# Performance work log

Measured on AMD Instinct MI355X. Metric: run time of the kernel, lower is better.

Reference implementation:

```python
import math
import jax, jax.numpy as jnp
import numpy as np

SEQ_LEN = 2048
PATCH = 16
D_MODEL = 512
N_HEADS = 8
D_FF = 2048
E_LAYERS = 3
KERNELS = (8, 4, 2, 1)


def _pos_embedding(L, d):
    # standard sinusoidal PE, matches PositionalEmbedding
    pos = np.arange(L, dtype=np.float32)[:, None]
    div = np.exp(np.arange(0, d, 2, dtype=np.float32) * (-math.log(10000.0) / d))
    pe = np.zeros((L, d), dtype=np.float32)
    pe[:, 0::2] = np.sin(pos * div)
    pe[:, 1::2] = np.cos(pos * div)
    return jnp.asarray(pe)


def _layer_norm(x, g, b, eps=1e-5):
    mu = jnp.mean(x, axis=-1, keepdims=True)
    var = jnp.mean(jnp.square(x - mu), axis=-1, keepdims=True)
    return (x - mu) * jax.lax.rsqrt(var + eps) * g + b


def setup_inputs() -> dict:
    key = jax.random.key(0)
    ks = jax.random.split(key, 12)
    bs, c = 8, 32
    s = 0.02
    L, D = E_LAYERS, D_MODEL
    inp = {
        "x_enc": jax.random.normal(ks[0], (bs, SEQ_LEN, c), jnp.float32),
        "W_emb": jax.random.normal(ks[1], (PATCH, D), jnp.float32) * s,
        "Wq": jax.random.normal(ks[2], (L, D, D), jnp.float32) * s,
        "bq": jnp.zeros((L, D), jnp.float32),
        "Wk": jax.random.normal(ks[3], (L, D, D), jnp.float32) * s,
        "bk": jnp.zeros((L, D), jnp.float32),
        "Wv": jax.random.normal(ks[4], (L, D, D), jnp.float32) * s,
        "bv": jnp.zeros((L, D), jnp.float32),
        "Wo": jax.random.normal(ks[5], (L, D, D), jnp.float32) * s,
        "bo": jnp.zeros((L, D), jnp.float32),
        "ln1_g": jnp.ones((L, D), jnp.float32),
        "ln1_b": jnp.zeros((L, D), jnp.float32),
        "W1": jax.random.normal(ks[6], (L, D, D_FF), jnp.float32) * s,
        "b1": jnp.zeros((L, D_FF), jnp.float32),
        "W2": jax.random.normal(ks[7], (L, D_FF, D), jnp.float32) * s,
        "b2": jnp.zeros((L, D), jnp.float32),
        "ln2_g": jnp.ones((L, D), jnp.float32),
        "ln2_b": jnp.zeros((L, D), jnp.float32),
        "lnf_g": jnp.ones((D,), jnp.float32),
        "lnf_b": jnp.zeros((D,), jnp.float32),
    }
    return inp


def reference(x_enc, W_emb, Wq, bq, Wk, bk, Wv, bv, Wo, bo,
              ln1_g, ln1_b, W1, b1, W2, b2, ln2_g, ln2_b, lnf_g, lnf_b):
    bs, t, c = x_enc.shape
    B = bs * c
    # channel-independent sequences: (bs, t, c) -> (bs*c, t)
    x = jnp.transpose(x_enc, (0, 2, 1)).reshape(B, t)

    # multi-scale interval sampling + patch embedding per scale
    p_lens = [(t // k) // PATCH for k in KERNELS]  # [16, 32, 64, 128]
    toks = []
    for k in KERNELS:
        xs = x[:, ::k]  # interval sampling (replicate-pad unfold [...,0] == stride-k sampling here)
        patches = xs.reshape(B, -1, PATCH)  # non-overlapping patches (stride == patch_len)
        toks.append(patches @ W_emb)  # value embedding, no bias
    h = jnp.concatenate(toks, axis=1)  # (B, L_tot=240, D)

    # multi-scale positional embedding: downsample pe of finest scale
    pe = _pos_embedding(p_lens[-1], D_MODEL)
    pos = jnp.concatenate([pe[::k] for k in KERNELS], axis=0)  # (240, D)
    h = h + pos[None]

    # block-diagonal scale-independence mask
    seg = np.concatenate([np.full(pl, i, dtype=np.int32) for i, pl in enumerate(p_lens)])
    allowed = jnp.asarray(seg[:, None] == seg[None, :])  # (240, 240) True = attend

    hd = D_MODEL // N_HEADS
    scale = 1.0 / math.sqrt(hd)
    Ltot = h.shape[1]
    for i in range(E_LAYERS):
        q = (h @ Wq[i] + bq[i]).reshape(B, Ltot, N_HEADS, hd)
        k_ = (h @ Wk[i] + bk[i]).reshape(B, Ltot, N_HEADS, hd)
        v_ = (h @ Wv[i] + bv[i]).reshape(B, Ltot, N_HEADS, hd)
        scores = jnp.einsum('blhd,bmhd->bhlm', q, k_) * scale
        scores = jnp.where(allowed[None, None], scores, -jnp.inf)
        attn = jax.nn.softmax(scores, axis=-1)
        o = jnp.einsum('bhlm,bmhd->blhd', attn, v_).reshape(B, Ltot, D_MODEL)
        o = o @ Wo[i] + bo[i]
        h = _layer_norm(h + o, ln1_g[i], ln1_b[i])
        f = jax.nn.gelu(h @ W1[i] + b1[i]) @ W2[i] + b2[i]
        h = _layer_norm(h + f, ln2_g[i], ln2_b[i])
    return _layer_norm(h, lnf_g, lnf_b)
```

## Files before the change

kernel.cpp:

```cpp
#include <hip/hip_runtime.h>
#include <hip/hip_bf16.h>

typedef short bf16x8 __attribute__((ext_vector_type(8)));
typedef float f32x4 __attribute__((ext_vector_type(4)));
using bf16 = __hip_bfloat16;

#define GLOBAL_LOAD_LDS16(g, l)                                                          \
    __builtin_amdgcn_global_load_lds((const __attribute__((address_space(1))) unsigned int*)(g), \
                                     (__attribute__((address_space(3))) unsigned int*)(l), \
                                     16, 0, 0)

static __device__ __forceinline__ float gelu_f(float x) {
    float u = 1.5957691216057308f * x * (1.0f + 0.044715f * x * x);
    return x / (1.0f + __expf(-u));
}

static __device__ __forceinline__ unsigned pack_bf16(float lo, float hi) {
    union { bf16 h; unsigned short u; } a, b;
    a.h = __float2bfloat16(lo);
    b.h = __float2bfloat16(hi);
    return ((unsigned)b.u << 16) | (unsigned)a.u;
}

static __device__ __forceinline__ int eperm(int r) {
    return (r & 1) | (((r >> 2) & 3) << 1) | (((r >> 1) & 1) << 3);
}

__global__ __launch_bounds__(256) void transpose_f32_bf16(const float* __restrict__ in,
                                                          bf16* __restrict__ out,
                                                          int R, int C, size_t zso) {
    __shared__ float tile[32][33];
    size_t zi = (size_t)blockIdx.z * R * C;
    size_t zo = (size_t)blockIdx.z * zso;
    int c0 = blockIdx.x * 32, r0 = blockIdx.y * 32;
    int tx = threadIdx.x & 31, ty = threadIdx.x >> 5;
    #pragma unroll
    for (int i = 0; i < 32; i += 8) {
        int r = r0 + ty + i, c = c0 + tx;
        if (r < R && c < C) tile[ty + i][tx] = in[zi + (size_t)r * C + c];
    }
    __syncthreads();
    #pragma unroll
    for (int i = 0; i < 32; i += 8) {
        int c = c0 + ty + i, r = r0 + tx;
        if (c < C && r < R) out[zo + (size_t)c * R + r] = __float2bfloat16(tile[tx][ty + i]);
    }
}

__global__ __launch_bounds__(256) void concat_bias(const float* __restrict__ bq,
                                                   const float* __restrict__ bk,
                                                   const float* __restrict__ bv,
                                                   float* __restrict__ out) {
    int i = blockIdx.x * 256 + threadIdx.x;
    if (i < 3 * 1536) {
        int L = i / 1536, r = i - L * 1536;
        float v = (r < 512) ? bq[L * 512 + r]
                : (r < 1024) ? bk[L * 512 + r - 512]
                             : bv[L * 512 + r - 1024];
        out[i] = v;
    }
}

__global__ __launch_bounds__(256) void transpose_v(const bf16* __restrict__ in,
                                                   bf16* __restrict__ out) {
    __shared__ bf16 tile[32][33];
    int b = blockIdx.z;
    int d0 = blockIdx.x * 32, t0 = blockIdx.y * 32;
    int tx = threadIdx.x & 31, ty = threadIdx.x >> 5;
    #pragma unroll
    for (int i = 0; i < 32; i += 8) {
        int tt = t0 + ty + i, dd = d0 + tx;
        if (tt < 240) tile[ty + i][tx] = in[((size_t)b * 240 + tt) * 1536 + 1024 + dd];
    }
    __syncthreads();
    #pragma unroll
    for (int i = 0; i < 32; i += 8) {
        int dd = d0 + ty + i, tt = t0 + tx;
        if (tt < 240) out[((size_t)b * 512 + dd) * 240 + tt] = tile[tx][ty + i];
    }
}

__global__ __launch_bounds__(256) void embed_kernel(const float* __restrict__ x_enc,
                                                    const float* __restrict__ W_emb,
                                                    bf16* __restrict__ h) {
    int row = blockIdx.x;
    int b = row / 240, l = row - b * 240;
    int s = (l < 16) ? 0 : (l < 48) ? 1 : (l < 112) ? 2 : 3;
    int len = 16 << s;
    int off = len - 16;
    int kk = 8 >> s;
    int j = l - off;
    int bs_i = b >> 5, c_i = b & 31;
    __shared__ float xv[16];
    int t = threadIdx.x;
    if (t < 16) {
        int tau = (j * 16 + t) * kk;
        xv[t] = x_enc[((size_t)bs_i * 2048 + tau) * 32 + c_i];
    }
    __syncthreads();
    int pe_row = j * kk;
    const float NEG2LN = -0.035977892078032f;
    for (int d = t; d < 512; d += 256) {
        float acc = 0.f;
        #pragma unroll
        for (int i = 0; i < 16; ++i) acc += xv[i] * W_emb[i * 512 + d];
        int di = d >> 1;
        float ang = (float)pe_row * expf((float)di * NEG2LN);
        float pos = (d & 1) ? cosf(ang) : sinf(ang);
        h[(size_t)row * 512 + d] = __float2bfloat16(acc + pos);
    }
}

__global__ __launch_bounds__(256) void gemm_bt(const bf16* __restrict__ A,
                                               const bf16* __restrict__ Bt,
                                               const float* __restrict__ bias,
                                               bf16* __restrict__ C,
                                               int M, int N, int K, int act) {
    __shared__ __align__(16) bf16 smem[2 * 128 * 64];
    bf16* As = smem;
    bf16* Bs = smem + 128 * 64;
    const int t = threadIdx.x;
    const int wave = t >> 6, lane = t & 63;
    const int quad = lane >> 4, l16 = lane & 15;

    const int nwg = gridDim.x * gridDim.y;
    const int id = blockIdx.y * gridDim.x + blockIdx.x;
    const int swzb = (id & 7) * (nwg >> 3) + (id >> 3);
    const int bx = swzb % gridDim.x, by = swzb / gridDim.x;
    const int m0 = by * 128, n0 = bx * 128;
    const int wm = (wave >> 1) * 64, wn = (wave & 1) * 64;

    f32x4 acc[4][4];
    #pragma unroll
    for (int a = 0; a < 4; ++a)
        #pragma unroll
        for (int b = 0; b < 4; ++b)
            #pragma unroll
            for (int r = 0; r < 4; ++r) acc[a][b][r] = 0.0f;

    const int srow = lane >> 3;
    const int schunk = (lane & 7) ^ srow;
    const bf16* Abase = A + (size_t)(m0 + wave * 32 + srow) * K + schunk * 8;
    const bf16* Bbase = Bt + (size_t)(n0 + wave * 32 + srow) * K + schunk * 8;

    for (int k0 = 0; k0 < K; k0 += 64) {
        __syncthreads();
        #pragma unroll
        for (int p = 0; p < 4; ++p) {
            GLOBAL_LOAD_LDS16(Abase + (size_t)p * 8 * K + k0, As + (wave * 4 + p) * 512);
            GLOBAL_LOAD_LDS16(Bbase + (size_t)p * 8 * K + k0, Bs + (wave * 4 + p) * 512);
        }
        __syncthreads();
        #pragma unroll
        for (int kt = 0; kt < 2; ++kt) {
            bf16x8 af[4], bfr[4];
            #pragma unroll
            for (int mi = 0; mi < 4; ++mi) {
                int row = wm + mi * 16 + l16;
                af[mi] = *(const bf16x8*)(&As[row * 64 + (((kt << 2) + quad) ^ (l16 & 7)) * 8]);
            }
            #pragma unroll
            for (int ni = 0; ni < 4; ++ni) {
                int row = wn + ni * 16 + l16;
                bfr[ni] = *(const bf16x8*)(&Bs[row * 64 + (((kt << 2) + quad) ^ (l16 & 7)) * 8]);
            }
            #pragma unroll
            for (int mi = 0; mi < 4; ++mi)
                #pragma unroll
                for (int ni = 0; ni < 4; ++ni)
                    acc[mi][ni] = __builtin_amdgcn_mfma_f32_16x16x32_bf16(af[mi], bfr[ni],
                                                                         acc[mi][ni], 0, 0, 0);
        }
    }

    __syncthreads();
    {
        char* ctile = (char*)smem;
        const int oddl = l16 & 1;
        #pragma unroll
        for (int ni = 0; ni < 4; ++ni) {
            int colt = wn + ni * 16 + l16;
            float bv = bias[n0 + colt];
            #pragma unroll
            for (int mi = 0; mi < 4; ++mi) {
                float v0 = acc[mi][ni][0] + bv;
                float v1 = acc[mi][ni][1] + bv;
                float v2 = acc[mi][ni][2] + bv;
                float v3 = acc[mi][ni][3] + bv;
                if (act) {
                    v0 = gelu_f(v0); v1 = gelu_f(v1);
                    v2 = gelu_f(v2); v3 = gelu_f(v3);
                }
                float p0 = __shfl_xor(v0, 1);
                float p1 = __shfl_xor(v1, 1);
                float p2 = __shfl_xor(v2, 1);
                float p3 = __shfl_xor(v3, 1);
                float lo0 = oddl ? p1 : v0, hi0 = oddl ? v1 : p0;
                float lo1 = oddl ? p3 : v2, hi1 = oddl ? v3 : p2;
                int rowt0 = wm + mi * 16 + quad * 4 + oddl;
                int rowt1 = rowt0 + 2;
                int colp = colt & ~1;
                int ch = colp >> 3;
                *(unsigned*)(ctile + rowt0 * 256 + (((ch ^ eperm(rowt0)) << 4) | ((colp & 7) << 1)))
                    = pack_bf16(lo0, hi0);
                *(unsigned*)(ctile + rowt1 * 256 + (((ch ^ eperm(rowt1)) << 4) | ((colp & 7) << 1)))
                    = pack_bf16(lo1, hi1);
            }
        }
        __syncthreads();
        const int rsub = t >> 4;
        const int cch = t & 15;
        #pragma unroll
        for (int g = 0; g < 8; ++g) {
            int row = g * 16 + rsub;
            bf16x8 v = *(const bf16x8*)(ctile + row * 256 + ((cch ^ eperm(row)) << 4));
            *(bf16x8*)(C + (size_t)(m0 + row) * N + n0 + cch * 8) = v;
        }
    }
}

template<int LEN>
__global__ __launch_bounds__(256) void attn_mfma(const bf16* __restrict__ qkv,
                                                 const bf16* __restrict__ vt,
                                                 bf16* __restrict__ o) {
    constexpr int NT = LEN / 16;
    constexpr int KT = (LEN >= 32) ? (LEN / 32) : 1;
    constexpr int PST = (LEN == 16) ? 40 : (LEN + 8);
    constexpr int SLABS = LEN / 16;
    constexpr int OFF = LEN - 16;
    __shared__ __align__(16) bf16 Plds[4 * 16 * PST];

    const int t = threadIdx.x;
    const int wave = t >> 6, lane = t & 63;
    const int quad = lane >> 4, l16 = lane & 15;
    const int task = blockIdx.x * 4 + wave;
    const int b = task / (8 * SLABS);
    const int rem = task - b * (8 * SLABS);
    const int h = rem / SLABS;
    const int slab = rem - h * SLABS;

    const size_t qbase = ((size_t)b * 240 + OFF) * 1536 + h * 64;
    const size_t obase = ((size_t)b * 240 + OFF) * 512 + h * 64;

    const bf16* qp = qkv + qbase + (size_t)(slab * 16 + l16) * 1536 + quad * 8;
    bf16x8 qf0 = *(const bf16x8*)qp;
    bf16x8 qf1 = *(const bf16x8*)(qp + 32);

    f32x4 sacc[NT];
    #pragma unroll
    for (int nt = 0; nt < NT; ++nt) {
        const bf16* kp = qkv + qbase + 512 + (size_t)(nt * 16 + l16) * 1536 + quad * 8;
        bf16x8 kf0 = *(const bf16x8*)kp;
        bf16x8 kf1 = *(const bf16x8*)(kp + 32);
        f32x4 a = {0.f, 0.f, 0.f, 0.f};
        a = __builtin_amdgcn_mfma_f32_16x16x32_bf16(qf0, kf0, a, 0, 0, 0);
        a = __builtin_amdgcn_mfma_f32_16x16x32_bf16(qf1, kf1, a, 0, 0, 0);
        sacc[nt] = a;
    }

    float mx[4], sm[4];
    #pragma unroll
    for (int r = 0; r < 4; ++r) mx[r] = -3.0e38f;
    #pragma unroll
    for (int nt = 0; nt < NT; ++nt)
        #pragma unroll
        for (int r = 0; r < 4; ++r) {
            sacc[nt][r] *= 0.125f;
            mx[r] = fmaxf(mx[r], sacc[nt][r]);
        }
    #pragma unroll
    for (int msk = 1; msk < 16; msk <<= 1)
        #pragma unroll
        for (int r = 0; r < 4; ++r) mx[r] = fmaxf(mx[r], __shfl_xor(mx[r], msk));
    #pragma unroll
    for (int r = 0; r < 4; ++r) sm[r] = 0.f;
    #pragma unroll
    for (int nt = 0; nt < NT; ++nt)
        #pragma unroll
        for (int r = 0; r < 4; ++r) {
            float p = __expf(sacc[nt][r] - mx[r]);
            sacc[nt][r] = p;
            sm[r] += p;
        }
    #pragma unroll
    for (int msk = 1; msk < 16; msk <<= 1)
        #pragma unroll
        for (int r = 0; r < 4; ++r) sm[r] += __shfl_xor(sm[r], msk);
    float inv[4];
    #pragma unroll
    for (int r = 0; r < 4; ++r) inv[r] = 1.f / sm[r];

    bf16* pw = Plds + wave * 16 * PST;
    #pragma unroll
    for (int nt = 0; nt < NT; ++nt)
        #pragma unroll
        for (int r = 0; r < 4; ++r)
            pw[(quad * 4 + r) * PST + nt * 16 + l16] =
                __float2bfloat16(sacc[nt][r] * inv[r]);
    if (LEN == 16) {
        #pragma unroll
        for (int r = 0; r < 4; ++r)
            pw[(quad * 4 + r) * PST + 16 + l16] = __float2bfloat16(0.f);
    }
    __syncthreads();

    f32x4 oacc[4];
    #pragma unroll
    for (int n4 = 0; n4 < 4; ++n4) {
        f32x4 z = {0.f, 0.f, 0.f, 0.f};
        oacc[n4] = z;
    }
    #pragma unroll
    for (int kt = 0; kt < KT; ++kt) {
        bf16x8 pf = *(const bf16x8*)&pw[l16 * PST + kt * 32 + quad * 8];
        #pragma unroll
        for (int n4 = 0; n4 < 4; ++n4) {
            const bf16* vp = vt + ((size_t)b * 512 + h * 64 + n4 * 16 + l16) * 240
                              + OFF + kt * 32 + quad * 8;
            bf16x8 vf = *(const bf16x8*)vp;
            oacc[n4] = __builtin_amdgcn_mfma_f32_16x16x32_bf16(pf, vf, oacc[n4], 0, 0, 0);
        }
    }
    #pragma unroll
    for (int n4 = 0; n4 < 4; ++n4)
        #pragma unroll
        for (int r = 0; r < 4; ++r)
            o[obase + (size_t)(slab * 16 + quad * 4 + r) * 512 + n4 * 16 + l16] =
                __float2bfloat16(oacc[n4][r]);
}

__global__ __launch_bounds__(256) void ln_kernel(const bf16* x, const bf16* res,
                                                 const float* __restrict__ g,
                                                 const float* __restrict__ bta,
                                                 bf16* out_bf, float* out_f) {
    int row = blockIdx.x;
    int t = threadIdx.x;
    const bf16* xr = x + (size_t)row * 512;
    float v0 = __bfloat162float(xr[t]);
    float v1 = __bfloat162float(xr[t + 256]);
    if (res) {
        const bf16* rr = res + (size_t)row * 512;
        v0 += __bfloat162float(rr[t]);
        v1 += __bfloat162float(rr[t + 256]);
    }
    float s = v0 + v1, ss = v0 * v0 + v1 * v1;
    #pragma unroll
    for (int mk = 1; mk < 64; mk <<= 1) { s += __shfl_xor(s, mk); ss += __shfl_xor(ss, mk); }
    __shared__ float red[8];
    int wave = t >> 6, lane = t & 63;
    if (lane == 0) { red[wave * 2] = s; red[wave * 2 + 1] = ss; }
    __syncthreads();
    s = red[0] + red[2] + red[4] + red[6];
    ss = red[1] + red[3] + red[5] + red[7];
    float mu = s * (1.f / 512.f);
    float var = ss * (1.f / 512.f) - mu * mu;
    float inv = rsqrtf(var + 1e-5f);
    float y0 = (v0 - mu) * inv * g[t] + bta[t];
    float y1 = (v1 - mu) * inv * g[t + 256] + bta[t + 256];
    if (out_bf) {
        bf16* orow = out_bf + (size_t)row * 512;
        orow[t] = __float2bfloat16(y0);
        orow[t + 256] = __float2bfloat16(y1);
    } else {
        float* orow = out_f + (size_t)row * 512;
        orow[t] = y0;
        orow[t + 256] = y1;
    }
}

extern "C" void kernel_launch(void* const* d_in, const int* in_sizes, int n_in,
                              void* d_out, int out_size, void* d_ws, size_t ws_size,
                              hipStream_t stream) {
    const float* x_enc = (const float*)d_in[0];
    const float* W_emb = (const float*)d_in[1];
    const float* Wq    = (const float*)d_in[2];
    const float* bq    = (const float*)d_in[3];
    const float* Wk    = (const float*)d_in[4];
    const float* bk    = (const float*)d_in[5];
    const float* Wv    = (const float*)d_in[6];
    const float* bv    = (const float*)d_in[7];
    const float* Wo    = (const float*)d_in[8];
    const float* bo    = (const float*)d_in[9];
    const float* ln1_g = (const float*)d_in[10];
    const float* ln1_b = (const float*)d_in[11];
    const float* W1    = (const float*)d_in[12];
    const float* b1    = (const float*)d_in[13];
    const float* W2    = (const float*)d_in[14];
    const float* b2    = (const float*)d_in[15];
    const float* ln2_g = (const float*)d_in[16];
    const float* ln2_b = (const float*)d_in[17];
    const float* lnf_g = (const float*)d_in[18];
    const float* lnf_b = (const float*)d_in[19];

    const int ROWS = 256 * 240;
    char* ws = (char*)d_ws;
    const size_t Hb = (size_t)ROWS * 512 * 2;
    bf16* h    = (bf16*)(ws);
    bf16* qkv  = (bf16*)(ws + Hb);
    bf16* oa   = (bf16*)(ws + 4 * Hb);
    bf16* scr2 = (bf16*)(ws + 5 * Hb);
    bf16* mid  = qkv;
    bf16* WqkvT = (bf16*)(ws + 6 * Hb);
    bf16* WoT  = WqkvT + (size_t)3 * 1536 * 512;
    bf16* W1T  = WoT + (size_t)3 * 512 * 512;
    bf16* W2T  = W1T + (size_t)3 * 512 * 2048;
    float* bcat = (float*)(W2T + (size_t)3 * 2048 * 512);

    bf16* vt     = scr2;
    bf16* oproj  = scr2;
    bf16* ffnout = scr2;

    dim3 blk(256);
    transpose_f32_bf16<<<dim3(16, 16, 3), blk, 0, stream>>>(Wq, WqkvT, 512, 512, (size_t)1536 * 512);
    transpose_f32_bf16<<<dim3(16, 16, 3), blk, 0, stream>>>(Wk, WqkvT + (size_t)512 * 512, 512, 512, (size_t)1536 * 512);
    transpose_f32_bf16<<<dim3(16, 16, 3), blk, 0, stream>>>(Wv, WqkvT + (size_t)1024 * 512, 512, 512, (size_t)1536 * 512);
    transpose_f32_bf16<<<dim3(16, 16, 3), blk, 0, stream>>>(Wo, WoT, 512, 512, (size_t)512 * 512);
    transpose_f32_bf16<<<dim3(64, 16, 3), blk, 0, stream>>>(W1, W1T, 512, 2048, (size_t)512 * 2048);
    transpose_f32_bf16<<<dim3(16, 64, 3), blk, 0, stream>>>(W2, W2T, 2048, 512, (size_t)2048 * 512);
    concat_bias<<<18, blk, 0, stream>>>(bq, bk, bv, bcat);

    embed_kernel<<<ROWS, blk, 0, stream>>>(x_enc, W_emb, h);

    for (int L = 0; L < 3; ++L) {
        size_t wo = (size_t)L * 512 * 512;
        size_t w1o = (size_t)L * 512 * 2048;
        gemm_bt<<<dim3(12, 480), blk, 0, stream>>>(h, WqkvT + (size_t)L * 1536 * 512,
                                                   bcat + L * 1536, qkv, ROWS, 1536, 512, 0);
        transpose_v<<<dim3(16, 8, 256), blk, 0, stream>>>(qkv, vt);
        attn_mfma<16><<<512, blk, 0, stream>>>(qkv, vt, oa);
        attn_mfma<32><<<1024, blk, 0, stream>>>(qkv, vt, oa);
        attn_mfma<64><<<2048, blk, 0, stream>>>(qkv, vt, oa);
        attn_mfma<128><<<4096, blk, 0, stream>>>(qkv, vt, oa);
        gemm_bt<<<dim3(4, 480), blk, 0, stream>>>(oa, WoT + wo, bo + L * 512, oproj, ROWS, 512, 512, 0);
        ln_kernel<<<ROWS, blk, 0, stream>>>(h, oproj, ln1_g + L * 512, ln1_b + L * 512, h, nullptr);
        gemm_bt<<<dim3(16, 480), blk, 0, stream>>>(h, W1T + w1o, b1 + L * 2048, mid, ROWS, 2048, 512, 1);
        gemm_bt<<<dim3(4, 480), blk, 0, stream>>>(mid, W2T + w1o, b2 + L * 512, ffnout, ROWS, 512, 2048, 0);
        ln_kernel<<<ROWS, blk, 0, stream>>>(h, ffnout, ln2_g + L * 512, ln2_b + L * 512, h, nullptr);
    }
    ln_kernel<<<ROWS, blk, 0, stream>>>(h, nullptr, lnf_g, lnf_b, nullptr, (float*)d_out);
}
```

Baseline: 2.875 ms.

## Replace GEMM with 256x256-tile, 8-wave kernel using 4-stage async LDS pipeline

Swaps the 128x128 single-buffered GEMM for a 256x256 tile kernel with 512 threads. Each wave computes a 128x64 sub-tile. K is walked in 32-wide slices through a four-slot LDS ring, with prefetch three tiles ahead and vmcnt-based waits. This replaces the full barrier round-trips per K step. The goal is to hide global load latency and raise data reuse per tile. In exchange it uses more accumulator registers and 128KB of LDS, which may limit occupancy. It also relies on ROWS being a multiple of 256.

```diff
diff --git a/kernel.cpp b/kernel.cpp
--- a/kernel.cpp
+++ b/kernel.cpp
@@ -20,10 +20,6 @@
     a.h = __float2bfloat16(lo);
     b.h = __float2bfloat16(hi);
     return ((unsigned)b.u << 16) | (unsigned)a.u;
-}
-
-static __device__ __forceinline__ int eperm(int r) {
-    return (r & 1) | (((r >> 2) & 3) << 1) | (((r >> 1) & 1) << 3);
 }
 
 __global__ __launch_bounds__(256) void transpose_f32_bf16(const float* __restrict__ in,
@@ -111,69 +107,84 @@
     }
 }
 
-__global__ __launch_bounds__(256) void gemm_bt(const bf16* __restrict__ A,
-                                               const bf16* __restrict__ Bt,
-                                               const float* __restrict__ bias,
-                                               bf16* __restrict__ C,
-                                               int M, int N, int K, int act) {
-    __shared__ __align__(16) bf16 smem[2 * 128 * 64];
-    bf16* As = smem;
-    bf16* Bs = smem + 128 * 64;
+__global__ __launch_bounds__(512, 2) void gemm_bt_256(const bf16* __restrict__ A,
+                                                      const bf16* __restrict__ Bt,
+                                                      const float* __restrict__ bias,
+                                                      bf16* __restrict__ C,
+                                                      int M, int N, int K, int act) {
+    __shared__ __align__(16) bf16 smem[4 * 16384];
     const int t = threadIdx.x;
     const int wave = t >> 6, lane = t & 63;
     const int quad = lane >> 4, l16 = lane & 15;
 
     const int nwg = gridDim.x * gridDim.y;
     const int id = blockIdx.y * gridDim.x + blockIdx.x;
-    const int swzb = (id & 7) * (nwg >> 3) + (id >> 3);
-    const int bx = swzb % gridDim.x, by = swzb / gridDim.x;
-    const int m0 = by * 128, n0 = bx * 128;
-    const int wm = (wave >> 1) * 64, wn = (wave & 1) * 64;
-
-    f32x4 acc[4][4];
-    #pragma unroll
-    for (int a = 0; a < 4; ++a)
+    const int swz = (id & 7) * (nwg >> 3) + (id >> 3);
+    const int bx = swz % gridDim.x, by = swz / gridDim.x;
+    const int m0 = by * 256, n0 = bx * 256;
+
+    const int wm = (wave >> 2) * 128;
+    const int wn = (wave & 3) * 64;
+
+    f32x4 acc[8][4];
+    #pragma unroll
+    for (int a = 0; a < 8; ++a)
         #pragma unroll
         for (int b = 0; b < 4; ++b)
             #pragma unroll
             for (int r = 0; r < 4; ++r) acc[a][b][r] = 0.0f;
 
-    const int srow = lane >> 3;
-    const int schunk = (lane & 7) ^ srow;
+    const int srow = lane >> 2;
+    const int schunk = (lane & 3) ^ (srow & 3);
     const bf16* Abase = A + (size_t)(m0 + wave * 32 + srow) * K + schunk * 8;
     const bf16* Bbase = Bt + (size_t)(n0 + wave * 32 + srow) * K + schunk * 8;
-
-    for (int k0 = 0; k0 < K; k0 += 64) {
-        __syncthreads();
-        #pragma unroll
-        for (int p = 0; p < 4; ++p) {
-            GLOBAL_LOAD_LDS16(Abase + (size_t)p * 8 * K + k0, As + (wave * 4 + p) * 512);
-            GLOBAL_LOAD_LDS16(Bbase + (size_t)p * 8 * K + k0, Bs + (wave * 4 + p) * 512);
-        }
-        __syncthreads();
-        #pragma unroll
-        for (int kt = 0; kt < 2; ++kt) {
-            bf16x8 af[4], bfr[4];
+    const int dst0 = wave * 1024 + lane * 8;
+
+#define STAGE_TILE(kt_, slot_)                                                          \
+    {                                                                                   \
+        bf16* Ad = smem + (slot_) * 16384;                                              \
+        const size_t ko = (size_t)(kt_) * 32;                                           \
+        GLOBAL_LOAD_LDS16(Abase + ko,                    Ad + dst0);                    \
+        GLOBAL_LOAD_LDS16(Abase + (size_t)16 * K + ko,   Ad + dst0 + 512);              \
+        GLOBAL_LOAD_LDS16(Bbase + ko,                    Ad + 8192 + dst0);             \
+        GLOBAL_LOAD_LDS16(Bbase + (size_t)16 * K + ko,   Ad + 8192 + dst0 + 512);       \
+    }
+
+    const int NK = K >> 5;
+    STAGE_TILE(0, 0);
+    STAGE_TILE(1, 1);
+    STAGE_TILE(2, 2);
+
+    const int rsw = (quad ^ (l16 & 3)) << 3;
+
+    for (int kt = 0; kt < NK; ++kt) {
+        const bf16* As = smem + (kt & 3) * 16384;
+        const bf16* Bs = As + 8192;
+        if (kt + 3 < NK) STAGE_TILE(kt + 3, (kt + 3) & 3);
+        const int rem = NK - 1 - kt;
+        if (rem >= 3)      asm volatile("s_waitcnt vmcnt(12)" ::: "memory");
+        else if (rem == 2) asm volatile("s_waitcnt vmcnt(8)" ::: "memory");
+        else if (rem == 1) asm volatile("s_waitcnt vmcnt(4)" ::: "memory");
+        else               asm volatile("s_waitcnt vmcnt(0)" ::: "memory");
+        asm volatile("s_barrier" ::: "memory");
+
+        bf16x8 af[8], bq[4];
+        #pragma unroll
+        for (int mi = 0; mi < 8; ++mi)
+            af[mi] = *(const bf16x8*)&As[(wm + mi * 16 + l16) * 32 + rsw];
+        #pragma unroll
+        for (int ni = 0; ni < 4; ++ni)
+            bq[ni] = *(const bf16x8*)&Bs[(wn + ni * 16 + l16) * 32 + rsw];
+        #pragma unroll
+        for (int mi = 0; mi < 8; ++mi)
             #pragma unroll
-            for (int mi = 0; mi < 4; ++mi) {
-                int row = wm + mi * 16 + l16;
-                af[mi] = *(const bf16x8*)(&As[row * 64 + (((kt << 2) + quad) ^ (l16 & 7)) * 8]);
-            }
-            #pragma unroll
-            for (int ni = 0; ni < 4; ++ni) {
-                int row = wn + ni * 16 + l16;
-                bfr[ni] = *(const bf16x8*)(&Bs[row * 64 + (((kt << 2) + quad) ^ (l16 & 7)) * 8]);
-            }
-            #pragma unroll
-            for (int mi = 0; mi < 4; ++mi)
-                #pragma unroll
-                for (int ni = 0; ni < 4; ++ni)
-                    acc[mi][ni] = __builtin_amdgcn_mfma_f32_16x16x32_bf16(af[mi], bfr[ni],
-                                                                         acc[mi][ni], 0, 0, 0);
-        }
-    }
-
-    __syncthreads();
+            for (int ni = 0; ni < 4; ++ni)
+                acc[mi][ni] = __builtin_amdgcn_mfma_f32_16x16x32_bf16(af[mi], bq[ni],
+                                                                     acc[mi][ni], 0, 0, 0);
+        asm volatile("s_barrier" ::: "memory");
+    }
+#undef STAGE_TILE
+
     {
         char* ctile = (char*)smem;
         const int oddl = l16 & 1;
@@ -182,7 +193,7 @@
             int colt = wn + ni * 16 + l16;
             float bv = bias[n0 + colt];
             #pragma unroll
-            for (int mi = 0; mi < 4; ++mi) {
+            for (int mi = 0; mi < 8; ++mi) {
                 float v0 = acc[mi][ni][0] + bv;
                 float v1 = acc[mi][ni][1] + bv;
                 float v2 = acc[mi][ni][2] + bv;
@@ -200,20 +211,19 @@
                 int rowt0 = wm + mi * 16 + quad * 4 + oddl;
                 int rowt1 = rowt0 + 2;
                 int colp = colt & ~1;
-                int ch = colp >> 3;
-                *(unsigned*)(ctile + rowt0 * 256 + (((ch ^ eperm(rowt0)) << 4) | ((colp & 7) << 1)))
+                *(unsigned*)(ctile + rowt0 * 512 + ((((colp >> 3) ^ (rowt0 & 31)) << 4) | ((colp & 7) << 1)))
                     = pack_bf16(lo0, hi0);
-                *(unsigned*)(ctile + rowt1 * 256 + (((ch ^ eperm(rowt1)) << 4) | ((colp & 7) << 1)))
+                *(unsigned*)(ctile + rowt1 * 512 + ((((colp >> 3) ^ (rowt1 & 31)) << 4) | ((colp & 7) << 1)))
                     = pack_bf16(lo1, hi1);
             }
         }
         __syncthreads();
-        const int rsub = t >> 4;
-        const int cch = t & 15;
-        #pragma unroll
-        for (int g = 0; g < 8; ++g) {
+        const int rsub = t >> 5;
+        const int cch = t & 31;
+        #pragma unroll
+        for (int g = 0; g < 16; ++g) {
             int row = g * 16 + rsub;
-            bf16x8 v = *(const bf16x8*)(ctile + row * 256 + ((cch ^ eperm(row)) << 4));
+            bf16x8 v = *(const bf16x8*)(ctile + row * 512 + ((cch ^ (row & 31)) << 4));
             *(bf16x8*)(C + (size_t)(m0 + row) * N + n0 + cch * 8) = v;
         }
     }
@@ -411,6 +421,7 @@
     bf16* ffnout = scr2;
 
     dim3 blk(256);
+    dim3 gblk(512);
     transpose_f32_bf16<<<dim3(16, 16, 3), blk, 0, stream>>>(Wq, WqkvT, 512, 512, (size_t)1536 * 512);
     transpose_f32_bf16<<<dim3(16, 16, 3), blk, 0, stream>>>(Wk, WqkvT + (size_t)512 * 512, 512, 512, (size_t)1536 * 512);
     transpose_f32_bf16<<<dim3(16, 16, 3), blk, 0, stream>>>(Wv, WqkvT + (size_t)1024 * 512, 512, 512, (size_t)1536 * 512);
@@ -424,17 +435,17 @@
     for (int L = 0; L < 3; ++L) {
         size_t wo = (size_t)L * 512 * 512;
         size_t w1o = (size_t)L * 512 * 2048;
-        gemm_bt<<<dim3(12, 480), blk, 0, stream>>>(h, WqkvT + (size_t)L * 1536 * 512,
-                                                   bcat + L * 1536, qkv, ROWS, 1536, 512, 0);
+        gemm_bt_256<<<dim3(6, 240), gblk, 0, stream>>>(h, WqkvT + (size_t)L * 1536 * 512,
+                                                       bcat + L * 1536, qkv, ROWS, 1536, 512, 0);
         transpose_v<<<dim3(16, 8, 256), blk, 0, stream>>>(qkv, vt);
         attn_mfma<16><<<512, blk, 0, stream>>>(qkv, vt, oa);
         attn_mfma<32><<<1024, blk, 0, stream>>>(qkv, vt, oa);
         attn_mfma<64><<<2048, blk, 0, stream>>>(qkv, vt, oa);
         attn_mfma<128><<<4096, blk, 0, stream>>>(qkv, vt, oa);
-        gemm_bt<<<dim3(4, 480), blk, 0, stream>>>(oa, WoT + wo, bo + L * 512, oproj, ROWS, 512, 512, 0);
+        gemm_bt_256<<<dim3(2, 240), gblk, 0, stream>>>(oa, WoT + wo, bo + L * 512, oproj, ROWS, 512, 512, 0);
         ln_kernel<<<ROWS, blk, 0, stream>>>(h, oproj, ln1_g + L * 512, ln1_b + L * 512, h, nullptr);
-        gemm_bt<<<dim3(16, 480), blk, 0, stream>>>(h, W1T + w1o, b1 + L * 2048, mid, ROWS, 2048, 512, 1);
-        gemm_bt<<<dim3(4, 480), blk, 0, stream>>>(mid, W2T + w1o, b2 + L * 512, ffnout, ROWS, 512, 2048, 0);
+        gemm_bt_256<<<dim3(8, 240), gblk, 0, stream>>>(h, W1T + w1o, b1 + L * 2048, mid, ROWS, 2048, 512, 1);
+        gemm_bt_256<<<dim3(2, 240), gblk, 0, stream>>>(mid, W2T + w1o, b2 + L * 512, ffnout, ROWS, 512, 2048, 0);
         ln_kernel<<<ROWS, blk, 0, stream>>>(h, ffnout, ln2_g + L * 512, ln2_b + L * 512, h, nullptr);
     }
     ln_kernel<<<ROWS, blk, 0, stream>>>(h, nullptr, lnf_g, lnf_b, nullptr, (float*)d_out);
```

New measurement: 2.995 ms. 1.04x slower.
